# Kernel optimization log

Measured on AMD Instinct MI355X. Metric: run time of the kernel, lower is better.

Reference implementation:

```python
import jax, jax.numpy as jnp
import numpy as np

B_GRAPHS, N_PER, T = 64, 5, 256
F_NODE, F_GLOB = 64, 16
H_MSG, H_UPD, H_GRP, H_ACT = 128, 128, 64, 4


def _lstm(x, Wih, Whh, bih, bhh):
    """PyTorch-semantics single-layer LSTM, batch_first=False.
    x: [L, B, Din] -> out [L, B, H]. Scan runs over dim 0 (faithful to the
    original code, which feeds [edges/nodes, T, F] into nn.LSTM)."""
    H = Whh.shape[1]
    xz = jnp.einsum('lbd,gd->lbg', x, Wih) + (bih + bhh)  # precomputed input proj [L,B,4H]
    h0 = jnp.zeros((x.shape[1], H), x.dtype)

    def step(carry, zt):
        h, c = carry
        z = zt + h @ Whh.T
        i, f, g, o = jnp.split(z, 4, axis=-1)  # torch gate order: i,f,g,o
        c = jax.nn.sigmoid(f) * c + jax.nn.sigmoid(i) * jnp.tanh(g)
        h = jax.nn.sigmoid(o) * jnp.tanh(c)
        return (h, c), h

    _, ys = jax.lax.scan(step, (h0, h0), xz)
    return ys


def _forward(nodes, global_attr,
             Wih_m, Whh_m, bih_m, bhh_m,
             Wih_u, Whh_u, bih_u, bhh_u,
             Wih_g, Whh_g, bih_g, bhh_g,
             Wih_a, Whh_a, bih_a, bhh_a,
             edge_indices, num_nodes, num_edges, batch_indices, chosen_who):
    N, Tdim = nodes.shape[0], nodes.shape[1]
    E = edge_indices.shape[1]
    B = num_nodes.shape[0]
    # Faithful to source: both src and target use edge_indices[0]
    src = edge_indices[0]
    tgt = edge_indices[0]
    ga = global_attr.reshape(-1, Tdim, global_attr.shape[1])  # [B, T, G]

    # --- message phase: gather -> LSTM -> relu -> scatter_min ---
    glob_e = jnp.repeat(ga, num_edges, axis=0, total_repeat_length=E)  # [E,T,G]
    msg_in = jnp.concatenate([nodes[src], nodes[tgt], glob_e], axis=2)  # [E,T,2F+G]
    message = jax.nn.relu(_lstm(msg_in, Wih_m, Whh_m, bih_m, bhh_m))    # [E,T,Hm]
    aggr = jax.ops.segment_min(message, tgt, num_segments=N)            # [N,T,Hm]

    # --- node update ---
    glob_n = jnp.repeat(ga, num_nodes, axis=0, total_repeat_length=N)   # [N,T,G]
    upd_in = jnp.concatenate([nodes, aggr, glob_n], axis=2)
    upd = jax.nn.relu(_lstm(upd_in, Wih_u, Whh_u, bih_u, bhh_u))        # [N,T,Hu]

    # --- global / group embedding ---
    agg_nodes = jax.ops.segment_min(upd, batch_indices, num_segments=B) # [B,T,Hu]
    group = jax.nn.relu(_lstm(jnp.concatenate([agg_nodes, ga], axis=2),
                              Wih_g, Whh_g, bih_g, bhh_g))              # [B,T,Hg]

    # --- action head ---
    agg_all = jax.ops.segment_min(upd, batch_indices, num_segments=B)
    counts = jax.ops.segment_sum(jnp.ones_like(batch_indices), batch_indices, num_segments=B)
    offsets = jnp.concatenate([jnp.zeros((1,), counts.dtype), jnp.cumsum(counts)[:-1]])
    adj = jnp.where(chosen_who == 3, chosen_who - 1, chosen_who)
    # faithful: element 0 is NOT adjusted/offset in the original loop
    atbw = jnp.where(jnp.arange(B) == 0, chosen_who, adj + offsets)
    chosen = upd[atbw]                                                  # [B,T,Hu]
    chosen = jnp.where((chosen_who == 3)[:, None, None], agg_all, chosen)
    act_in = jnp.concatenate([chosen, group], axis=2)                   # [B,T,Hu+Hg]
    res = _lstm(act_in, Wih_a, Whh_a, bih_a, bhh_a)[:, -1, :]           # [B, A]
    return jax.nn.softmax(res, axis=1)


def _lstm_params(k, din, h):
    k1, k2, k3, k4 = jax.random.split(k, 4)
    s = 1.0 / np.sqrt(h)
    return (jax.random.uniform(k1, (4 * h, din), jnp.float32, -s, s),
            jax.random.uniform(k2, (4 * h, h), jnp.float32, -s, s),
            jax.random.uniform(k3, (4 * h,), jnp.float32, -s, s),
            jax.random.uniform(k4, (4 * h,), jnp.float32, -s, s))


def setup_inputs() -> dict:
    key = jax.random.key(0)
    ks = jax.random.split(key, 8)
    N = B_GRAPHS * N_PER
    # complete directed graph inside each small group
    src, dst = [], []
    for g in range(B_GRAPHS):
        for i in range(N_PER):
            for j in range(N_PER):
                if i != j:
                    src.append(g * N_PER + i)
                    dst.append(g * N_PER + j)
    edge_indices = jnp.array([src, dst], dtype=jnp.int32)
    inp = {
        'nodes': jax.random.normal(ks[0], (N, T, F_NODE), jnp.float32),
        'global_attr': jax.random.normal(ks[1], (B_GRAPHS * T, F_GLOB), jnp.float32),
        'edge_indices': edge_indices,
        'num_nodes': jnp.full((B_GRAPHS,), N_PER, jnp.int32),
        'num_edges': jnp.full((B_GRAPHS,), N_PER * (N_PER - 1), jnp.int32),
        'batch_indices': jnp.repeat(jnp.arange(B_GRAPHS, dtype=jnp.int32), N_PER),
        'chosen_who': jax.random.randint(ks[2], (B_GRAPHS,), 0, 4, jnp.int32),
    }
    names = [('m', 2 * F_NODE + F_GLOB, H_MSG), ('u', H_MSG + F_NODE + F_GLOB, H_UPD),
             ('g', H_UPD + F_GLOB, H_GRP), ('a', H_UPD + H_GRP, H_ACT)]
    for idx, (suf, din, h) in enumerate(names):
        Wih, Whh, bih, bhh = _lstm_params(ks[3 + idx], din, h)
        inp['Wih_' + suf] = Wih
        inp['Whh_' + suf] = Whh
        inp['bih_' + suf] = bih
        inp['bhh_' + suf] = bhh
    return inp


def reference(nodes, global_attr, edge_indices, num_nodes, num_edges, batch_indices, chosen_who,
              Wih_m, Whh_m, bih_m, bhh_m, Wih_u, Whh_u, bih_u, bhh_u,
              Wih_g, Whh_g, bih_g, bhh_g, Wih_a, Whh_a, bih_a, bhh_a):
    return _forward(nodes, global_attr,
                    Wih_m, Whh_m, bih_m, bhh_m,
                    Wih_u, Whh_u, bih_u, bhh_u,
                    Wih_g, Whh_g, bih_g, bhh_g,
                    Wih_a, Whh_a, bih_a, bhh_a,
                    edge_indices, num_nodes, num_edges, batch_indices, chosen_who)
```

## Files before the change

kernel.cpp:

```cpp
#include <hip/hip_runtime.h>

typedef unsigned int u32;
typedef unsigned short u16;
typedef __fp16 h2 __attribute__((ext_vector_type(2)));

#define BG 64
#define NNODE 320
#define NEDGE 1280
#define TT 256
#define FN 64
#define FG 16
#define HM 128
#define HU 128
#define HG 64
#define HA 4
#define ZM 512
#define ZU 512
#define ZG 256
#define ZA 16
#define DM 144
#define DU 208
#define DG 144
#define DA 192

#define CV 64
#define O_NODES 0
#define O_GA    20480
#define O_WM    21504
#define O_WHM   95232
#define O_BM    160768
#define O_WU    161280
#define O_WHU   267776
#define O_BU    333312
#define O_WG    333824
#define O_WHG   370688
#define O_BG2   387072
#define O_WA    387328
#define O_WHA   390400
#define O_BA    390464
#define CONV_TOTAL 390480
#define O_XZM   390528
#define O_XZU   (O_XZM + NEDGE * ZM)
#define O_XZG   (O_XZU + NNODE * ZU)
#define O_XZA   (O_XZG + BG * ZG)
#define O_AGGR  (O_XZA + BG * ZA)
#define O_AGGB  (O_AGGR + NNODE * HM)
#define O_UPD   (O_AGGB + BG * HU)
#define WS_FLOATS (CV + O_UPD + NNODE * HU)

__device__ __forceinline__ float bf2f(u16 v) {
  return __uint_as_float(((u32)v) << 16);
}
__device__ __forceinline__ float rcp_(float x) { return __builtin_amdgcn_rcpf(x); }
__device__ __forceinline__ float sigf(float x) { return rcp_(1.0f + __expf(-x)); }
__device__ __forceinline__ float tanh_(float x) {
  float e = __expf(-2.0f * fabsf(x));
  float t = (1.0f - e) * rcp_(1.0f + e);
  return copysignf(t, x);
}
__device__ __forceinline__ float cvt(const void* p, int i, int flag) {
  return flag ? bf2f(((const u16*)p)[i]) : ((const float*)p)[i];
}

__device__ __forceinline__ h2 pk2(float a, float b) {
  return __builtin_amdgcn_cvt_pkrtz(a, b);
}
__device__ __forceinline__ u32 pk2u(float a, float b) {
  h2 r = __builtin_amdgcn_cvt_pkrtz(a, b);
  u32 out;
  __builtin_memcpy(&out, &r, 4);
  return out;
}

__device__ __forceinline__ float fdot2_(h2 a, h2 b, float c) {
#if __has_builtin(__builtin_amdgcn_fdot2)
  return __builtin_amdgcn_fdot2(a, b, c, false);
#else
  u32 ua, ub;
  __builtin_memcpy(&ua, &a, 4);
  __builtin_memcpy(&ub, &b, 4);
  asm("v_dot2_f32_f16 %0, %1, %2, %0" : "+v"(c) : "v"(ua), "v"(ub));
  return c;
#endif
}

template <int CTRL>
__device__ __forceinline__ float dppmov(float s) {
  return __int_as_float(
      __builtin_amdgcn_update_dpp(0, __float_as_int(s), CTRL, 0xF, 0xF, true));
}

#define BAR() asm volatile("s_waitcnt lgkmcnt(0)\n\ts_barrier" ::: "memory")

__global__ void k_detect(const u32* __restrict__ raw, int* __restrict__ flagp) {
  const int t = threadIdx.x;
  int zlo = 0, hits = 0;
  for (int k = t; k < 256; k += 64) {
    u32 w = raw[k];
    if ((w & 0xFFFFu) == 0u) zlo++;
    u32 m = (w >> 8) & 0x7Fu;
    if (m >= 40u && m <= 70u) hits++;
  }
#pragma unroll
  for (int off = 32; off; off >>= 1) {
    zlo += __shfl_down(zlo, off, 64);
    hits += __shfl_down(hits, off, 64);
  }
  if (t == 0) *flagp = (zlo < 128 && hits >= 128) ? 1 : 0;
}

__global__ __launch_bounds__(256) void k_convert(
    const void* nodes, const void* gattr,
    const void* Wm, const void* Whm, const void* bm1, const void* bm2,
    const void* Wu, const void* Whu, const void* bu1, const void* bu2,
    const void* Wg, const void* Whg, const void* bg1, const void* bg2,
    const void* Wa, const void* Wha, const void* ba1, const void* ba2,
    const int* __restrict__ flagp, float* __restrict__ dst) {
  const int flag = *flagp;
  const int i = blockIdx.x * 256 + threadIdx.x;
  if (i >= CONV_TOTAL) return;
  float v;
  if (i < O_GA) {
    int n = i >> 6, f = i & 63;
    v = cvt(nodes, (n * TT + (TT - 1)) * FN + f, flag);
  } else if (i < O_WM) {
    int l = i - O_GA; int b = l >> 4, g = l & 15;
    v = cvt(gattr, (b * TT + (TT - 1)) * FG + g, flag);
  } else if (i < O_BM) {
    v = (i < O_WHM) ? cvt(Wm, i - O_WM, flag) : cvt(Whm, i - O_WHM, flag);
  } else if (i < O_WU) {
    int l = i - O_BM; v = cvt(bm1, l, flag) + cvt(bm2, l, flag);
  } else if (i < O_BU) {
    v = (i < O_WHU) ? cvt(Wu, i - O_WU, flag) : cvt(Whu, i - O_WHU, flag);
  } else if (i < O_WG) {
    int l = i - O_BU; v = cvt(bu1, l, flag) + cvt(bu2, l, flag);
  } else if (i < O_BG2) {
    v = (i < O_WHG) ? cvt(Wg, i - O_WG, flag) : cvt(Whg, i - O_WHG, flag);
  } else if (i < O_WA) {
    int l = i - O_BG2; v = cvt(bg1, l, flag) + cvt(bg2, l, flag);
  } else if (i < O_WHA) {
    v = cvt(Wa, i - O_WA, flag);
  } else if (i < O_BA) {
    v = cvt(Wha, i - O_WHA, flag);
  } else {
    int l = i - O_BA; v = cvt(ba1, l, flag) + cvt(ba2, l, flag);
  }
  dst[i] = v;
}

__global__ __launch_bounds__(256) void k_pre(
    const float* __restrict__ cva,
    const int* __restrict__ eidx, const int* __restrict__ num_nodes,
    const int* __restrict__ num_edges,
    float* __restrict__ XZm, float* __restrict__ XZu, float* __restrict__ XZg) {
  const int blk = blockIdx.x, tid = threadIdx.x;
  __shared__ float xv[FN];
  __shared__ float gav[FG];
  __shared__ int sgr;
  const float* nodes255 = cva + O_NODES;
  const float* ga255 = cva + O_GA;

  if (blk < NEDGE) {
    const int e = blk;
    if (tid == 0) {
      int g = 0, acc = 0;
      while (g < BG) { int c = num_edges[g]; if (e < acc + c) break; acc += c; ++g; }
      if (g >= BG) g = BG - 1;
      sgr = g;
    }
    const int srcn = eidx[e];
    if (tid < FN) xv[tid] = nodes255[srcn * FN + tid];
    __syncthreads();
    if (tid < FG) gav[tid] = ga255[sgr * FG + tid];
    __syncthreads();
    for (int j = tid; j < ZM; j += 256) {
      const float* wr = cva + O_WM + j * DM;
      float acc = cva[O_BM + j];
#pragma unroll
      for (int d = 0; d < FN; ++d) acc += (wr[d] + wr[FN + d]) * xv[d];
#pragma unroll
      for (int d = 0; d < FG; ++d) acc += wr[2 * FN + d] * gav[d];
      XZm[(size_t)e * ZM + j] = acc;
    }
  } else if (blk < NEDGE + NNODE) {
    const int n = blk - NEDGE;
    if (tid == 0) {
      int g = 0, acc = 0;
      while (g < BG) { int c = num_nodes[g]; if (n < acc + c) break; acc += c; ++g; }
      if (g >= BG) g = BG - 1;
      sgr = g;
    }
    if (tid < FN) xv[tid] = nodes255[n * FN + tid];
    __syncthreads();
    if (tid < FG) gav[tid] = ga255[sgr * FG + tid];
    __syncthreads();
    for (int j = tid; j < ZU; j += 256) {
      const float* wr = cva + O_WU + j * DU;
      float acc = cva[O_BU + j];
#pragma unroll
      for (int d = 0; d < FN; ++d) acc += wr[d] * xv[d];
#pragma unroll
      for (int d = 0; d < FG; ++d) acc += wr[FN + HM + d] * gav[d];
      XZu[(size_t)n * ZU + j] = acc;
    }
  } else {
    const int b = blk - NEDGE - NNODE;
    if (tid < FG) gav[tid] = ga255[b * FG + tid];
    __syncthreads();
    if (tid < ZG) {
      const float* wr = cva + O_WG + tid * DG;
      float acc = cva[O_BG2 + tid];
#pragma unroll
      for (int d = 0; d < FG; ++d) acc += wr[HU + d] * gav[d];
      XZg[(size_t)b * ZG + tid] = acc;
    }
  }
}

template <int STEPS>
__global__ __launch_bounds__(1024, 4) void k_chain(
    const float* __restrict__ Whh, const float* __restrict__ XZ,
    float* __restrict__ hout) {
  const int lane = threadIdx.x & 63;
  const int wv = threadIdx.x >> 6;
  const int kc = lane & 7;
  const int grp = lane >> 3;
  const int elem = wv * 8 + grp;
  const int b2 = (lane >> 2) & 1;
  const int p = (lane & 3) ^ (3 * b2);
  const bool islead = ((lane & 7) == 0);
  __shared__ u32 hbuf[2][96];

  h2 w16[32];
#pragma unroll
  for (int pp = 0; pp < 4; ++pp) {
    const float4* wr =
        (const float4*)(Whh + (size_t)(pp * 128 + elem) * 128 + kc * 16);
#pragma unroll
    for (int q = 0; q < 4; ++q) {
      float4 t = wr[q];
      w16[pp * 8 + 2 * q] = pk2(t.x, t.y);
      w16[pp * 8 + 2 * q + 1] = pk2(t.z, t.w);
    }
  }
  const float LOG2E = 1.4426950408889634f;
  const float kmul = (p == 2) ? (-2.0f * LOG2E) : (-LOG2E);
  const float smul = (p == 2) ? 2.0f : 1.0f;
  const float badd = (p == 2) ? -1.0f : 0.0f;
  const float KT2 = -2.0f * LOG2E;

  if (threadIdx.x < 192) ((u32*)hbuf)[threadIdx.x] = 0u;
  float c = 0.0f;
  float hrelu_prev = 0.0f;
  float xz = XZ[p * 128 + elem];
  BAR();
  int cur = 0;
  for (int e = 0; e < STEPS; ++e) {
    const uint4* hb = (const uint4*)&hbuf[cur][kc * 12];
    uint4 ta = hb[0], tb = hb[1];
    u32 hraw[8] = {ta.x, ta.y, ta.z, ta.w, tb.x, tb.y, tb.z, tb.w};
    h2 hv[8];
#pragma unroll
    for (int k = 0; k < 8; ++k) __builtin_memcpy(&hv[k], &hraw[k], 4);
    float a0 = 0.0f, a1 = 0.0f, a2 = 0.0f, a3 = 0.0f;
#pragma unroll
    for (int k = 0; k < 8; ++k) {
      a0 = fdot2_(w16[0 * 8 + k], hv[k], a0);
      a1 = fdot2_(w16[1 * 8 + k], hv[k], a1);
      a2 = fdot2_(w16[2 * 8 + k], hv[k], a2);
      a3 = fdot2_(w16[3 * 8 + k], hv[k], a3);
    }
    const int sel0 = (lane & 1) ^ b2;
    const int sel1 = ((lane >> 1) & 1) ^ b2;
    float u0 = sel0 ? a1 : a0, d0 = sel0 ? a0 : a1;
    float u1 = sel0 ? a3 : a2, d1 = sel0 ? a2 : a3;
    u0 += dppmov<0xB1>(d0);
    u1 += dppmov<0xB1>(d1);
    float uu = sel1 ? u1 : u0, dd = sel1 ? u0 : u1;
    uu += dppmov<0x4E>(dd);
    uu += dppmov<0x141>(uu);
    float z = uu + xz;
    xz = XZ[(size_t)(e + 1) * 512 + p * 128 + elem];
    float ex = __builtin_amdgcn_exp2f(z * kmul);
    float gq = __builtin_fmaf(smul, rcp_(1.0f + ex), badd);
    float gf = dppmov<0xB1>(gq);
    float gt = dppmov<0x4E>(gq);
    float go = dppmov<0x1B>(gq);
    c = __builtin_fmaf(gf, c, gq * gt);
    float ec = __builtin_amdgcn_exp2f(c * KT2);
    float th = __builtin_fmaf(2.0f, rcp_(1.0f + ec), -1.0f);
    float h = go * th;
    if (islead) {
      u16* hwp = (u16*)(&hbuf[cur ^ 1][0]);
      hwp[(elem >> 4) * 24 + (elem & 15)] = (u16)pk2u(h, h);
      if (e > 0) hout[(size_t)(e - 1) * 128 + elem] = hrelu_prev;
      hrelu_prev = fmaxf(h, 0.0f);
    }
    BAR();
    cur ^= 1;
  }
  if (islead) hout[(size_t)(STEPS - 1) * 128 + elem] = hrelu_prev;
}

__global__ __launch_bounds__(256) void k_aggminproj(
    const float* __restrict__ cva, const float* __restrict__ msg,
    const int* __restrict__ eidx, float* __restrict__ XZu) {
  const int n = blockIdx.x, tid = threadIdx.x;
  __shared__ float av[HM];
  if (tid < HM) {
    float m = __uint_as_float(0x7f800000u);
    for (int e = 0; e < NEDGE; ++e) {
      if (eidx[e] == n) m = fminf(m, msg[(size_t)e * HM + tid]);
    }
    av[tid] = m;
  }
  __syncthreads();
  for (int j = tid; j < ZU; j += 256) {
    const float* wr = cva + O_WU + j * DU + FN;
    float acc = 0.0f;
#pragma unroll
    for (int k = 0; k < HM; ++k) acc += wr[k] * av[k];
    XZu[(size_t)n * ZU + j] += acc;
  }
}

__global__ __launch_bounds__(256) void k_gproj(
    const float* __restrict__ cva, const float* __restrict__ upd,
    const int* __restrict__ bidx, const int* __restrict__ who,
    float* __restrict__ XZg, float* __restrict__ XZa) {
  const int blk = blockIdx.x, tid = threadIdx.x;
  __shared__ float buf[HU];
  __shared__ int satbw;
  if (blk < BG) {
    const int b = blk;
    if (tid < HU) {
      float m = __uint_as_float(0x7f800000u);
      for (int n = 0; n < NNODE; ++n) {
        if (bidx[n] == b) m = fminf(m, upd[(size_t)n * HU + tid]);
      }
      buf[tid] = m;
    }
    __syncthreads();
    if (tid < ZG) {
      const float* wr = cva + O_WG + tid * DG;
      float acc = 0.0f;
#pragma unroll
      for (int k = 0; k < HU; ++k) acc += wr[k] * buf[k];
      XZg[(size_t)b * ZG + tid] += acc;
    }
  } else {
    const int b = blk - BG;
    const int whoB = who[b];
    if (tid == 0) {
      int off = 0;
      for (int i = 0; i < NNODE; ++i) off += (bidx[i] < b) ? 1 : 0;
      const int adj = (whoB == 3) ? 2 : whoB;
      satbw = (b == 0) ? who[0] : (adj + off);
    }
    if (whoB == 3) {
      if (tid < HU) {
        float m = __uint_as_float(0x7f800000u);
        for (int n = 0; n < NNODE; ++n) {
          if (bidx[n] == b) m = fminf(m, upd[(size_t)n * HU + tid]);
        }
        buf[tid] = m;
      }
      __syncthreads();
    } else {
      __syncthreads();
      if (tid < HU) buf[tid] = upd[(size_t)satbw * HU + tid];
      __syncthreads();
    }
    if (tid < ZA) {
      const float* wr = cva + O_WA + tid * DA;
      float acc = cva[O_BA + tid];
#pragma unroll
      for (int k = 0; k < HU; ++k) acc += wr[k] * buf[k];
      XZa[(size_t)b * ZA + tid] = acc;
    }
  }
}

__global__ __launch_bounds__(256, 2) void k_final(
    const float* __restrict__ cva, const float* __restrict__ XZg,
    const float* __restrict__ XZa, float* __restrict__ out) {
  const int j = threadIdx.x;
  __shared__ __align__(16) float hg[HG];
  __shared__ float zsg[ZG];
  __shared__ float grp[BG * HG];
  __shared__ float za[ZA];
  __shared__ float haL[HA];
  __shared__ float res[BG * HA];

  float wg[HG];
  {
    const float* wr = cva + O_WHG + j * HG;
#pragma unroll
    for (int k = 0; k < HG; ++k) wg[k] = wr[k];
  }
  if (j < HG) hg[j] = 0.0f;
  float cg = 0.0f;
  __syncthreads();
  for (int b = 0; b < BG; ++b) {
    float acc = XZg[(size_t)b * ZG + j];
#pragma unroll
    for (int k = 0; k < HG; ++k) acc += wg[k] * hg[k];
    zsg[j] = acc;
    __syncthreads();
    if (j < HG) {
      float zi = zsg[j], zf = zsg[HG + j], zg = zsg[2 * HG + j], zo = zsg[3 * HG + j];
      cg = sigf(zf) * cg + sigf(zi) * tanh_(zg);
      float h = sigf(zo) * tanh_(cg);
      hg[j] = h;
      grp[b * HG + j] = fmaxf(h, 0.0f);
    }
    __syncthreads();
  }

  float wa2[HG];
  float wha[HA];
  if (j < ZA) {
    const float* wr2 = cva + O_WA + j * DA + HU;
#pragma unroll
    for (int k = 0; k < HG; ++k) wa2[k] = wr2[k];
#pragma unroll
    for (int k = 0; k < HA; ++k) wha[k] = cva[O_WHA + j * HA + k];
  }
  if (j < HA) haL[j] = 0.0f;
  float ca = 0.0f;
  __syncthreads();
  for (int b = 0; b < BG; ++b) {
    if (j < ZA) {
      float acc = XZa[(size_t)b * ZA + j];
#pragma unroll
      for (int k = 0; k < HG; ++k) acc += wa2[k] * grp[b * HG + k];
#pragma unroll
      for (int k = 0; k < HA; ++k) acc += wha[k] * haL[k];
      za[j] = acc;
    }
    __syncthreads();
    if (j < HA) {
      float zi = za[j], zf = za[HA + j], zg = za[2 * HA + j], zo = za[3 * HA + j];
      ca = sigf(zf) * ca + sigf(zi) * tanh_(zg);
      float h = sigf(zo) * tanh_(ca);
      haL[j] = h;
      res[b * HA + j] = h;
    }
    __syncthreads();
  }
  if (j < BG) {
    float x0 = res[j * 4 + 0], x1 = res[j * 4 + 1];
    float x2 = res[j * 4 + 2], x3 = res[j * 4 + 3];
    float m = fmaxf(fmaxf(x0, x1), fmaxf(x2, x3));
    float e0 = __expf(x0 - m), e1 = __expf(x1 - m);
    float e2 = __expf(x2 - m), e3 = __expf(x3 - m);
    float s = e0 + e1 + e2 + e3;
    out[j * 4 + 0] = e0 / s;
    out[j * 4 + 1] = e1 / s;
    out[j * 4 + 2] = e2 / s;
    out[j * 4 + 3] = e3 / s;
  }
}

__global__ void k_zero(float* out) { out[threadIdx.x] = 0.0f; }

extern "C" void kernel_launch(void* const* d_in, const int* in_sizes, int n_in,
                              void* d_out, int out_size, void* d_ws, size_t ws_size,
                              hipStream_t stream) {
  const void* nodes = d_in[0];
  const void* gattr = d_in[1];
  const int* eidx  = (const int*)d_in[2];
  const int* nn    = (const int*)d_in[3];
  const int* ne    = (const int*)d_in[4];
  const int* bidx  = (const int*)d_in[5];
  const int* who   = (const int*)d_in[6];

  if (ws_size < (size_t)WS_FLOATS * 4) {
    k_zero<<<1, 256, 0, stream>>>((float*)d_out);
    return;
  }

  float* ws = (float*)d_ws;
  int* flagp = (int*)d_ws;
  float* cva = ws + CV;
  float* XZm = cva + O_XZM;
  float* XZu = cva + O_XZU;
  float* XZg = cva + O_XZG;
  float* XZa = cva + O_XZA;
  float* upd = cva + O_UPD;
  float* msg = XZm;

  k_detect<<<1, 64, 0, stream>>>((const u32*)nodes, flagp);
  k_convert<<<(CONV_TOTAL + 255) / 256, 256, 0, stream>>>(
      nodes, gattr,
      d_in[7], d_in[8], d_in[9], d_in[10],
      d_in[11], d_in[12], d_in[13], d_in[14],
      d_in[15], d_in[16], d_in[17], d_in[18],
      d_in[19], d_in[20], d_in[21], d_in[22],
      flagp, cva);
  k_pre<<<NEDGE + NNODE + BG, 256, 0, stream>>>(cva, eidx, nn, ne, XZm, XZu, XZg);
  k_chain<NEDGE><<<1, 1024, 0, stream>>>(cva + O_WHM, XZm, msg);
  k_aggminproj<<<NNODE, 256, 0, stream>>>(cva, msg, eidx, XZu);
  k_chain<NNODE><<<1, 1024, 0, stream>>>(cva + O_WHU, XZu, upd);
  k_gproj<<<2 * BG, 256, 0, stream>>>(cva, upd, bidx, who, XZg, XZa);
  k_final<<<1, 256, 0, stream>>>(cva, XZg, XZa, (float*)d_out);
}
```

Measured before the change: 1.293 ms.

## Restructure LSTM recurrence to one full-row dot per thread with broadcast h

```diff
diff --git a/kernel.cpp b/kernel.cpp
--- a/kernel.cpp
+++ b/kernel.cpp
@@ -218,29 +218,23 @@
 }
 
 template <int STEPS>
-__global__ __launch_bounds__(1024, 4) void k_chain(
+__global__ __launch_bounds__(512, 2) void k_chain(
     const float* __restrict__ Whh, const float* __restrict__ XZ,
     float* __restrict__ hout) {
-  const int lane = threadIdx.x & 63;
-  const int wv = threadIdx.x >> 6;
-  const int kc = lane & 7;
-  const int grp = lane >> 3;
-  const int elem = wv * 8 + grp;
-  const int b2 = (lane >> 2) & 1;
-  const int p = (lane & 3) ^ (3 * b2);
-  const bool islead = ((lane & 7) == 0);
-  __shared__ u32 hbuf[2][96];
-
-  h2 w16[32];
-#pragma unroll
-  for (int pp = 0; pp < 4; ++pp) {
-    const float4* wr =
-        (const float4*)(Whh + (size_t)(pp * 128 + elem) * 128 + kc * 16);
-#pragma unroll
-    for (int q = 0; q < 4; ++q) {
-      float4 t = wr[q];
-      w16[pp * 8 + 2 * q] = pk2(t.x, t.y);
-      w16[pp * 8 + 2 * q + 1] = pk2(t.z, t.w);
+  const int t = threadIdx.x;
+  const int p = t & 3;
+  const int elem = t >> 2;
+  const bool islead = (p == 0);
+  __shared__ u32 hbuf[2][80];
+
+  h2 w16[64];
+  {
+    const float4* wr = (const float4*)(Whh + (size_t)(p * 128 + elem) * 128);
+#pragma unroll
+    for (int q = 0; q < 32; ++q) {
+      float4 v = wr[q];
+      w16[2 * q] = pk2(v.x, v.y);
+      w16[2 * q + 1] = pk2(v.z, v.w);
     }
   }
   const float LOG2E = 1.4426950408889634f;
@@ -249,37 +243,29 @@
   const float badd = (p == 2) ? -1.0f : 0.0f;
   const float KT2 = -2.0f * LOG2E;
 
-  if (threadIdx.x < 192) ((u32*)hbuf)[threadIdx.x] = 0u;
+  if (t < 160) ((u32*)hbuf)[t] = 0u;
   float c = 0.0f;
   float hrelu_prev = 0.0f;
   float xz = XZ[p * 128 + elem];
   BAR();
   int cur = 0;
   for (int e = 0; e < STEPS; ++e) {
-    const uint4* hb = (const uint4*)&hbuf[cur][kc * 12];
-    uint4 ta = hb[0], tb = hb[1];
-    u32 hraw[8] = {ta.x, ta.y, ta.z, ta.w, tb.x, tb.y, tb.z, tb.w};
-    h2 hv[8];
-#pragma unroll
-    for (int k = 0; k < 8; ++k) __builtin_memcpy(&hv[k], &hraw[k], 4);
+    const uint4* hb = (const uint4*)&hbuf[cur][0];
     float a0 = 0.0f, a1 = 0.0f, a2 = 0.0f, a3 = 0.0f;
 #pragma unroll
-    for (int k = 0; k < 8; ++k) {
-      a0 = fdot2_(w16[0 * 8 + k], hv[k], a0);
-      a1 = fdot2_(w16[1 * 8 + k], hv[k], a1);
-      a2 = fdot2_(w16[2 * 8 + k], hv[k], a2);
-      a3 = fdot2_(w16[3 * 8 + k], hv[k], a3);
-    }
-    const int sel0 = (lane & 1) ^ b2;
-    const int sel1 = ((lane >> 1) & 1) ^ b2;
-    float u0 = sel0 ? a1 : a0, d0 = sel0 ? a0 : a1;
-    float u1 = sel0 ? a3 : a2, d1 = sel0 ? a2 : a3;
-    u0 += dppmov<0xB1>(d0);
-    u1 += dppmov<0xB1>(d1);
-    float uu = sel1 ? u1 : u0, dd = sel1 ? u0 : u1;
-    uu += dppmov<0x4E>(dd);
-    uu += dppmov<0x141>(uu);
-    float z = uu + xz;
+    for (int q = 0; q < 16; ++q) {
+      uint4 tv = hb[q];
+      h2 h0, h1, h2_, h3;
+      __builtin_memcpy(&h0, &tv.x, 4);
+      __builtin_memcpy(&h1, &tv.y, 4);
+      __builtin_memcpy(&h2_, &tv.z, 4);
+      __builtin_memcpy(&h3, &tv.w, 4);
+      a0 = fdot2_(w16[4 * q + 0], h0, a0);
+      a1 = fdot2_(w16[4 * q + 1], h1, a1);
+      a2 = fdot2_(w16[4 * q + 2], h2_, a2);
+      a3 = fdot2_(w16[4 * q + 3], h3, a3);
+    }
+    float z = ((a0 + a1) + (a2 + a3)) + xz;
     xz = XZ[(size_t)(e + 1) * 512 + p * 128 + elem];
     float ex = __builtin_amdgcn_exp2f(z * kmul);
     float gq = __builtin_fmaf(smul, rcp_(1.0f + ex), badd);
@@ -291,8 +277,7 @@
     float th = __builtin_fmaf(2.0f, rcp_(1.0f + ec), -1.0f);
     float h = go * th;
     if (islead) {
-      u16* hwp = (u16*)(&hbuf[cur ^ 1][0]);
-      hwp[(elem >> 4) * 24 + (elem & 15)] = (u16)pk2u(h, h);
+      ((u16*)&hbuf[cur ^ 1][0])[elem] = (u16)pk2u(h, h);
       if (e > 0) hout[(size_t)(e - 1) * 128 + elem] = hrelu_prev;
       hrelu_prev = fmaxf(h, 0.0f);
     }
@@ -499,9 +484,9 @@
       d_in[19], d_in[20], d_in[21], d_in[22],
       flagp, cva);
   k_pre<<<NEDGE + NNODE + BG, 256, 0, stream>>>(cva, eidx, nn, ne, XZm, XZu, XZg);
-  k_chain<NEDGE><<<1, 1024, 0, stream>>>(cva + O_WHM, XZm, msg);
+  k_chain<NEDGE><<<1, 512, 0, stream>>>(cva + O_WHM, XZm, msg);
   k_aggminproj<<<NNODE, 256, 0, stream>>>(cva, msg, eidx, XZu);
-  k_chain<NNODE><<<1, 1024, 0, stream>>>(cva + O_WHU, XZu, upd);
+  k_chain<NNODE><<<1, 512, 0, stream>>>(cva + O_WHU, XZu, upd);
   k_gproj<<<2 * BG, 256, 0, stream>>>(cva, upd, bidx, who, XZg, XZa);
   k_final<<<1, 256, 0, stream>>>(cva, XZg, XZa, (float*)d_out);
 }
```

Result: faster. 1.143 ms (-11.6%).
